# Kernel optimization log

Hardware: AMD Instinct MI355X
Metric: run time of the kernel (lower is better)

The kernel has to match this reference:

```python
import jax, jax.numpy as jnp
import numpy as np

D, H, L, E, K, FF, VIS, NC, NT = 1024, 8, 4, 4, 2, 2048, 1536, 4, 4
HD = D // H


def layer_norm(x, g, b, eps=1e-5):
    m = x.mean(-1, keepdims=True)
    v = ((x - m) ** 2).mean(-1, keepdims=True)
    return (x - m) / jnp.sqrt(v + eps) * g + b


def sinusoidal_pos(seq_len):
    pos = jnp.arange(seq_len, dtype=jnp.float32)[:, None]
    div = jnp.exp(jnp.arange(0, D, 2, dtype=jnp.float32) * (-jnp.log(10000.0) / D))
    pe = jnp.zeros((seq_len, D), dtype=jnp.float32)
    pe = pe.at[:, 0::2].set(jnp.sin(pos * div))
    pe = pe.at[:, 1::2].set(jnp.cos(pos * div))
    return pe


def mha(x, wi, bi, wo, bo):
    # wi: [D, 3D] (pre-transposed), wo: [D, D]
    B, S, _ = x.shape
    qkv = x @ wi + bi
    q, k, v = jnp.split(qkv, 3, axis=-1)
    split = lambda t: t.reshape(B, S, H, HD).transpose(0, 2, 1, 3)
    q, k, v = split(q), split(k), split(v)
    scores = jnp.einsum('bhqd,bhkd->bhqk', q, k) / jnp.sqrt(jnp.float32(HD))
    a = jax.nn.softmax(scores, axis=-1)
    o = jnp.einsum('bhqk,bhkd->bhqd', a, v).transpose(0, 2, 1, 3).reshape(B, S, D)
    return o @ wo + bo


def moe(x_flat, rw, rb, w1, b1, w2, b2):
    # x_flat: [N, D]; rw: [D, E]; w1: [E, D, FF]; w2: [E, FF, D]
    logits = x_flat @ rw + rb                      # [N, E]
    topv, topi = jax.lax.top_k(logits, K)          # [N, K]
    probs = jax.nn.softmax(topv, axis=-1)          # softmax over the top-k logits
    onehot = jax.nn.one_hot(topi, E, dtype=x_flat.dtype)      # [N, K, E]
    combine = jnp.einsum('nk,nke->ne', probs, onehot)         # [N, E]
    h = jax.nn.relu(jnp.einsum('nd,edf->enf', x_flat, w1) + b1[:, None, :])  # [E, N, FF]
    o = jnp.einsum('enf,efd->end', h, w2) + b2[:, None, :]                   # [E, N, D]
    return jnp.einsum('ne,end->nd', combine, o)


def setup_inputs() -> dict:
    key = jax.random.key(0)
    ks = iter(jax.random.split(key, 32))
    s = 0.02
    n = lambda shape: jax.random.normal(next(ks), shape, dtype=jnp.float32) * s
    inp = {
        'vis_feat': jax.random.normal(next(ks), (64, 128, VIS), dtype=jnp.float32),
        'proj_w': n((VIS, D)), 'proj_b': jnp.zeros((D,), jnp.float32),
        'in_proj_w': n((L, D, 3 * D)), 'in_proj_b': jnp.zeros((L, 3 * D), jnp.float32),
        'out_proj_w': n((L, D, D)), 'out_proj_b': jnp.zeros((L, D), jnp.float32),
        'ln1_g': jnp.ones((L, D), jnp.float32), 'ln1_b': jnp.zeros((L, D), jnp.float32),
        'ln2_g': jnp.ones((L, D), jnp.float32), 'ln2_b': jnp.zeros((L, D), jnp.float32),
        'router_w': n((L, D, E)), 'router_b': jnp.zeros((L, E), jnp.float32),
        'ew1': n((L, E, D, FF)), 'eb1': jnp.zeros((L, E, FF), jnp.float32),
        'ew2': n((L, E, FF, D)), 'eb2': jnp.zeros((L, E, D), jnp.float32),
        'attn_w': n((D, 1)), 'attn_b': jnp.zeros((1,), jnp.float32),
        'heads_w': n((NT, D, NC)), 'heads_b': jnp.zeros((NT, NC), jnp.float32),
    }
    return inp


def reference(vis_feat, proj_w, proj_b, in_proj_w, in_proj_b, out_proj_w, out_proj_b,
              ln1_g, ln1_b, ln2_g, ln2_b, router_w, router_b, ew1, eb1, ew2, eb2,
              attn_w, attn_b, heads_w, heads_b):
    B, S, _ = vis_feat.shape
    x = vis_feat @ proj_w + proj_b            # projection to d_model=1024
    x = x + sinusoidal_pos(S)[None]           # positional encoding
    for l in range(L):                         # 4 MoE transformer layers
        x = layer_norm(x + mha(x, in_proj_w[l], in_proj_b[l], out_proj_w[l], out_proj_b[l]),
                       ln1_g[l], ln1_b[l])
        moe_out = moe(x.reshape(B * S, D), router_w[l], router_b[l],
                      ew1[l], eb1[l], ew2[l], eb2[l]).reshape(B, S, D)
        x = layer_norm(x + moe_out, ln2_g[l], ln2_b[l])
    # attention pooling over time, then 4 task heads
    scores = jax.nn.softmax(x @ attn_w + attn_b, axis=1)   # [B, S, 1]
    pooled = jnp.sum(scores * x, axis=1)                   # [B, D]
    logits = jnp.einsum('bd,tdc->tbc', pooled, heads_w) + heads_b[:, None, :]  # [4, B, 4]
    return logits
```

## Files before the change

### kernel.cpp

```cpp
#include <hip/hip_runtime.h>
#include <hip/hip_bf16.h>

typedef unsigned short u16;
typedef unsigned int u32;
using short8 = __attribute__((ext_vector_type(8))) short;
using f32x4  = __attribute__((ext_vector_type(4))) float;

__device__ __forceinline__ u16 f2bu(float f) {
  u32 u = __builtin_bit_cast(u32, f);
  u32 r = u + 0x7fffu + ((u >> 16) & 1u);
  return (u16)(r >> 16);
}
__device__ __forceinline__ float bu2f(u16 u) {
  u32 x = ((u32)u) << 16;
  return __builtin_bit_cast(float, x);
}
__device__ __forceinline__ float waveRedSum(float v) {
  #pragma unroll
  for (int off = 32; off > 0; off >>= 1) v += __shfl_xor(v, off, 64);
  return v;
}
__device__ __forceinline__ void gload16(const void* g, void* l) {
  __builtin_amdgcn_global_load_lds((const __attribute__((address_space(1))) u32*)g,
                                   (__attribute__((address_space(3))) u32*)l, 16, 0, 0);
}

template<int MODE>
__global__ __launch_bounds__(256) void gemm_bt(
    const u16* __restrict__ A, const u16* __restrict__ Bt, const float* __restrict__ bias,
    float* __restrict__ Cf, u16* __restrict__ Cb, u16* __restrict__ M0, u16* __restrict__ M1,
    const int* __restrict__ tok, const float* __restrict__ prob, const int* __restrict__ slot,
    const int* __restrict__ poff, const int* __restrict__ cnts,
    int N, int K)
{
  const int gx = gridDim.x;
  const int nwg = gx * gridDim.y;
  int lid = blockIdx.y * gx + blockIdx.x;
  lid = (lid & 7) * (nwg >> 3) + (lid >> 3);
  const int brow = (lid / gx) << 7, bcol = (lid % gx) << 7;

  int e = 0, rowEnd = 0;
  const u16* Bw = Bt;
  const float* bw = bias;
  if constexpr (MODE >= 2) {
    if (brow >= poff[4]) return;
    #pragma unroll
    for (int q = 1; q < 4; ++q) if (brow >= poff[q]) e = q;
    rowEnd = poff[e] + cnts[e];
    Bw = Bt + (size_t)e * N * K;
    bw = bias + e * N;
  }

  __shared__ __align__(16) u16 As[128 * 32];
  __shared__ __align__(16) u16 Bs[128 * 32];
  const int tid = threadIdx.x;
  const int wave = tid >> 6, lane = tid & 63;
  const int wr = wave >> 1, wc = wave & 1;
  const int r = lane & 15, kg = lane >> 4;

  f32x4 acc[4][4];
  #pragma unroll
  for (int m = 0; m < 4; ++m)
    #pragma unroll
    for (int n = 0; n < 4; ++n) acc[m][n] = f32x4{0.f, 0.f, 0.f, 0.f};

  const int c0 = (wave << 6) + lane;
  const int row0 = c0 >> 2, col0 = (c0 & 3) << 3;
  const int c1 = 256 + c0;
  const int row1 = c1 >> 2, col1 = (c1 & 3) << 3;

  size_t ar0, ar1;
  if constexpr (MODE == 2) {
    const int g0 = brow + row0, g1 = brow + row1;
    ar0 = (size_t)tok[(g0 < rowEnd) ? g0 : poff[e]];
    ar1 = (size_t)tok[(g1 < rowEnd) ? g1 : poff[e]];
  } else {
    ar0 = (size_t)(brow + row0);
    ar1 = (size_t)(brow + row1);
  }
  const u16* Bb = Bw + (size_t)bcol * K;

  for (int k0 = 0; k0 < K; k0 += 32) {
    __syncthreads();
    gload16(A + ar0 * K + k0 + col0, &As[(wave << 6) * 8]);
    gload16(Bb + (size_t)row0 * K + k0 + col0, &Bs[(wave << 6) * 8]);
    gload16(A + ar1 * K + k0 + col1, &As[(256 + (wave << 6)) * 8]);
    gload16(Bb + (size_t)row1 * K + k0 + col1, &Bs[(256 + (wave << 6)) * 8]);
    __syncthreads();
    short8 a[4], b[4];
    #pragma unroll
    for (int m = 0; m < 4; ++m)
      a[m] = *(const short8*)&As[((wr << 6) + (m << 4) + r) * 32 + (kg << 3)];
    #pragma unroll
    for (int n = 0; n < 4; ++n)
      b[n] = *(const short8*)&Bs[((wc << 6) + (n << 4) + r) * 32 + (kg << 3)];
    #pragma unroll
    for (int m = 0; m < 4; ++m)
      #pragma unroll
      for (int n = 0; n < 4; ++n)
        acc[m][n] = __builtin_amdgcn_mfma_f32_16x16x32_bf16(a[m], b[n], acc[m][n], 0, 0, 0);
  }

  if constexpr (MODE == 3) {
    #pragma unroll
    for (int m = 0; m < 4; ++m) {
      #pragma unroll
      for (int i4 = 0; i4 < 4; ++i4) {
        const int row = brow + (wr << 6) + (m << 4) + (kg << 2) + i4;
        if (row < rowEnd) {
          const int t = tok[row];
          const float pp = prob[row];
          u16* dst = slot[row] ? M1 : M0;
          #pragma unroll
          for (int n = 0; n < 4; ++n) {
            const int col = bcol + (wc << 6) + (n << 4) + r;
            dst[(size_t)t * N + col] = f2bu((acc[m][n][i4] + bw[col]) * pp);
          }
        }
      }
    }
  } else {
    #pragma unroll
    for (int m = 0; m < 4; ++m) {
      #pragma unroll
      for (int n = 0; n < 4; ++n) {
        const int col = bcol + (wc << 6) + (n << 4) + r;
        const float bv = bw[col];
        #pragma unroll
        for (int i4 = 0; i4 < 4; ++i4) {
          const int row = brow + (wr << 6) + (m << 4) + (kg << 2) + i4;
          const float v = acc[m][n][i4] + bv;
          const size_t off = (size_t)row * N + col;
          if constexpr (MODE == 0) Cf[off] = v;
          else if constexpr (MODE == 1) Cb[off] = f2bu(v);
          else Cb[off] = f2bu(fmaxf(v, 0.f));
        }
      }
    }
  }
}

__global__ __launch_bounds__(256) void tconv_kernel(const float* __restrict__ src, u16* __restrict__ dst,
                                                    int K, int N)
{
  __shared__ float t[32][33];
  const size_t moff = (size_t)blockIdx.z * K * N;
  const float* s = src + moff;
  u16* d = dst + moff;
  const int n0 = blockIdx.x << 5, k0 = blockIdx.y << 5;
  const int x = threadIdx.x, y = threadIdx.y;
  #pragma unroll
  for (int j = 0; j < 4; ++j) t[y + 8 * j][x] = s[(size_t)(k0 + y + 8 * j) * N + n0 + x];
  __syncthreads();
  #pragma unroll
  for (int j = 0; j < 4; ++j) d[(size_t)(n0 + y + 8 * j) * K + k0 + x] = f2bu(t[x][y + 8 * j]);
}

__global__ __launch_bounds__(256) void conv_kernel(const float* __restrict__ in, u16* __restrict__ out)
{
  const size_t i = ((size_t)blockIdx.x * 256 + threadIdx.x) * 4;
  float4 v = *(const float4*)(in + i);
  *(ushort4*)(out + i) = make_ushort4(f2bu(v.x), f2bu(v.y), f2bu(v.z), f2bu(v.w));
}

__global__ __launch_bounds__(256) void pe_kernel(float* __restrict__ X, u16* __restrict__ Xb)
{
  const int idx = blockIdx.x * 256 + threadIdx.x;
  const int d = idx & 1023;
  const int s = (idx >> 10) & 127;
  const float de = (float)(d & ~1);
  const float ang = (float)s * expf(de * (-9.210340371976184f / 1024.f));
  const float pe = (d & 1) ? cosf(ang) : sinf(ang);
  const float v = X[idx] + pe;
  X[idx] = v;
  Xb[idx] = f2bu(v);
}

__global__ __launch_bounds__(256) void ln_kernel(const float* __restrict__ Xi, const float* __restrict__ R,
    const float* __restrict__ g, const float* __restrict__ be,
    float* __restrict__ Xo, u16* __restrict__ Xbo)
{
  const size_t base = (size_t)blockIdx.x << 10;
  const int tid = threadIdx.x;
  float vals[4]; float s = 0.f, s2 = 0.f;
  #pragma unroll
  for (int j = 0; j < 4; ++j) {
    const int d = tid + (j << 8);
    const float v = Xi[base + d] + R[base + d];
    vals[j] = v; s += v; s2 += v * v;
  }
  s = waveRedSum(s); s2 = waveRedSum(s2);
  __shared__ float rs[4], rs2[4];
  const int wave = tid >> 6, lane = tid & 63;
  if (lane == 0) { rs[wave] = s; rs2[wave] = s2; }
  __syncthreads();
  s = rs[0] + rs[1] + rs[2] + rs[3];
  s2 = rs2[0] + rs2[1] + rs2[2] + rs2[3];
  const float mean = s * (1.f / 1024.f);
  const float var = s2 * (1.f / 1024.f) - mean * mean;
  const float inv = rsqrtf(var + 1e-5f);
  #pragma unroll
  for (int j = 0; j < 4; ++j) {
    const int d = tid + (j << 8);
    const float y = (vals[j] - mean) * inv * g[d] + be[d];
    Xo[base + d] = y;
    Xbo[base + d] = f2bu(y);
  }
}

__global__ __launch_bounds__(256) void ln2_kernel(const float* __restrict__ Xi,
    const u16* __restrict__ R0, const u16* __restrict__ R1,
    const float* __restrict__ g, const float* __restrict__ be,
    float* __restrict__ Xo, u16* __restrict__ Xbo)
{
  const size_t base = (size_t)blockIdx.x << 10;
  const int tid = threadIdx.x;
  float vals[4]; float s = 0.f, s2 = 0.f;
  #pragma unroll
  for (int j = 0; j < 4; ++j) {
    const int d = tid + (j << 8);
    const float v = Xi[base + d] + (bu2f(R0[base + d]) + bu2f(R1[base + d]));
    vals[j] = v; s += v; s2 += v * v;
  }
  s = waveRedSum(s); s2 = waveRedSum(s2);
  __shared__ float rs[4], rs2[4];
  const int wave = tid >> 6, lane = tid & 63;
  if (lane == 0) { rs[wave] = s; rs2[wave] = s2; }
  __syncthreads();
  s = rs[0] + rs[1] + rs[2] + rs[3];
  s2 = rs2[0] + rs2[1] + rs2[2] + rs2[3];
  const float mean = s * (1.f / 1024.f);
  const float var = s2 * (1.f / 1024.f) - mean * mean;
  const float inv = rsqrtf(var + 1e-5f);
  #pragma unroll
  for (int j = 0; j < 4; ++j) {
    const int d = tid + (j << 8);
    const float y = (vals[j] - mean) * inv * g[d] + be[d];
    Xo[base + d] = y;
    Xbo[base + d] = f2bu(y);
  }
}

#define LDW 136
__global__ __launch_bounds__(256) void attn_mfma_kernel(const u16* __restrict__ QKVb, u16* __restrict__ ATTb)
{
  __shared__ __align__(16) u16 Kb[128 * LDW];
  __shared__ __align__(16) u16 Vt[128 * LDW];
  __shared__ __align__(16) u16 Pb[128 * LDW];
  const int b = blockIdx.x >> 3, h = blockIdx.x & 7;
  const int tid = threadIdx.x;
  const int wave = tid >> 6, lane = tid & 63;
  const int r = lane & 15, kg = lane >> 4;
  const u16* base = QKVb + (size_t)b * 128 * 3072 + h * 128;

  for (int i = tid; i < 128 * 16; i += 256) {
    const int row = i >> 4, c8 = (i & 15) << 3;
    *(short8*)&Kb[row * LDW + c8] = *(const short8*)(base + (size_t)row * 3072 + 1024 + c8);
  }
  for (int i = tid; i < 128 * 128; i += 256) {
    const int d = i & 127, key = i >> 7;
    Vt[d * LDW + key] = base[(size_t)key * 3072 + 2048 + d];
  }

  short8 a[2][4];
  #pragma unroll
  for (int m = 0; m < 2; ++m) {
    const int row = wave * 32 + m * 16 + r;
    const u16* qp = base + (size_t)row * 3072;
    #pragma unroll
    for (int ks = 0; ks < 4; ++ks)
      a[m][ks] = *(const short8*)(qp + ks * 32 + kg * 8);
  }
  __syncthreads();

  f32x4 acc[2][8];
  #pragma unroll
  for (int m = 0; m < 2; ++m)
    #pragma unroll
    for (int n = 0; n < 8; ++n) acc[m][n] = f32x4{0.f, 0.f, 0.f, 0.f};
  #pragma unroll
  for (int n = 0; n < 8; ++n) {
    #pragma unroll
    for (int ks = 0; ks < 4; ++ks) {
      short8 bf = *(const short8*)&Kb[(n * 16 + r) * LDW + ks * 32 + kg * 8];
      #pragma unroll
      for (int m = 0; m < 2; ++m)
        acc[m][n] = __builtin_amdgcn_mfma_f32_16x16x32_bf16(a[m][ks], bf, acc[m][n], 0, 0, 0);
    }
  }

  const float sc = 0.08838834764831845f;
  #pragma unroll
  for (int m = 0; m < 2; ++m) {
    #pragma unroll
    for (int i = 0; i < 4; ++i) {
      float mx = -1e30f;
      #pragma unroll
      for (int n = 0; n < 8; ++n) mx = fmaxf(mx, acc[m][n][i]);
      #pragma unroll
      for (int msk = 1; msk < 16; msk <<= 1) mx = fmaxf(mx, __shfl_xor(mx, msk, 64));
      float s = 0.f;
      #pragma unroll
      for (int n = 0; n < 8; ++n) { float pv = __expf((acc[m][n][i] - mx) * sc); acc[m][n][i] = pv; s += pv; }
      #pragma unroll
      for (int msk = 1; msk < 16; msk <<= 1) s += __shfl_xor(s, msk, 64);
      const float inv = 1.f / s;
      #pragma unroll
      for (int n = 0; n < 8; ++n) {
        const int prow = wave * 32 + m * 16 + kg * 4 + i;
        Pb[prow * LDW + n * 16 + r] = f2bu(acc[m][n][i] * inv);
      }
    }
  }

  f32x4 oacc[2][8];
  #pragma unroll
  for (int m = 0; m < 2; ++m)
    #pragma unroll
    for (int n = 0; n < 8; ++n) oacc[m][n] = f32x4{0.f, 0.f, 0.f, 0.f};
  #pragma unroll
  for (int ks = 0; ks < 4; ++ks) {
    short8 pa[2];
    #pragma unroll
    for (int m = 0; m < 2; ++m)
      pa[m] = *(const short8*)&Pb[(wave * 32 + m * 16 + r) * LDW + ks * 32 + kg * 8];
    #pragma unroll
    for (int n = 0; n < 8; ++n) {
      short8 vb = *(const short8*)&Vt[(n * 16 + r) * LDW + ks * 32 + kg * 8];
      #pragma unroll
      for (int m = 0; m < 2; ++m)
        oacc[m][n] = __builtin_amdgcn_mfma_f32_16x16x32_bf16(pa[m], vb, oacc[m][n], 0, 0, 0);
    }
  }

  u16* op = ATTb + ((size_t)b * 128) * 1024 + h * 128;
  #pragma unroll
  for (int m = 0; m < 2; ++m) {
    #pragma unroll
    for (int n = 0; n < 8; ++n) {
      #pragma unroll
      for (int i = 0; i < 4; ++i) {
        const int row = wave * 32 + m * 16 + kg * 4 + i;
        op[(size_t)row * 1024 + n * 16 + r] = f2bu(oacc[m][n][i]);
      }
    }
  }
}
#undef LDW

__global__ __launch_bounds__(256) void router_kernel(const float* __restrict__ X, const float* __restrict__ rw,
    const float* __restrict__ rb, int* __restrict__ choice, float* __restrict__ prob2)
{
  const int token = blockIdx.x * 4 + (threadIdx.x >> 6);
  const int lane = threadIdx.x & 63;
  const float* xp = X + ((size_t)token << 10);
  float a0 = 0, a1 = 0, a2 = 0, a3 = 0;
  #pragma unroll
  for (int j = 0; j < 16; ++j) {
    const int k = lane + (j << 6);
    const float x = xp[k];
    const float4 w = *(const float4*)(rw + ((size_t)k << 2));
    a0 += x * w.x; a1 += x * w.y; a2 += x * w.z; a3 += x * w.w;
  }
  a0 = waveRedSum(a0); a1 = waveRedSum(a1); a2 = waveRedSum(a2); a3 = waveRedSum(a3);
  if (lane == 0) {
    float v[4] = {a0 + rb[0], a1 + rb[1], a2 + rb[2], a3 + rb[3]};
    int i1 = 0;
    for (int e = 1; e < 4; ++e) if (v[e] > v[i1]) i1 = e;
    int i2 = (i1 == 0) ? 1 : 0;
    for (int e = 0; e < 4; ++e) if (e != i1 && v[e] > v[i2]) i2 = e;
    const float p2 = __expf(v[i2] - v[i1]);
    const float is = 1.f / (1.f + p2);
    choice[token] = i1 | (i2 << 8);
    prob2[token * 2]     = is;
    prob2[token * 2 + 1] = p2 * is;
  }
}

__global__ __launch_bounds__(256) void build_lists_kernel(
    const int* __restrict__ choice, const float* __restrict__ prob2,
    int* __restrict__ cnt, int* __restrict__ poff,
    int* __restrict__ tok, float* __restrict__ prob, int* __restrict__ slot)
{
  const int tid = threadIdx.x;
  __shared__ int sc[256];
  __shared__ int basev;
  if (tid == 0) basev = 0;
  __syncthreads();
  for (int e = 0; e < 4; ++e) {
    const int t0 = tid << 5;
    int code[32]; int mycount = 0;
    #pragma unroll
    for (int j = 0; j < 32; ++j) {
      const int c = choice[t0 + j];
      const int m = ((c & 255) == e) ? 1 : (((c >> 8) == e) ? 2 : 0);
      code[j] = m;
      mycount += (m != 0);
    }
    sc[tid] = mycount;
    __syncthreads();
    for (int off = 1; off < 256; off <<= 1) {
      const int add = (tid >= off) ? sc[tid - off] : 0;
      __syncthreads();
      sc[tid] += add;
      __syncthreads();
    }
    const int total = sc[255];
    const int start = basev;
    int pos = start + sc[tid] - mycount;
    #pragma unroll
    for (int j = 0; j < 32; ++j) {
      if (code[j]) {
        const int token = t0 + j;
        tok[pos] = token;
        prob[pos] = prob2[token * 2 + (code[j] - 1)];
        slot[pos] = code[j] - 1;
        ++pos;
      }
    }
    __syncthreads();
    if (tid == 0) {
      cnt[e] = total;
      poff[e] = start;
      basev = start + ((total + 255) & ~255);
      if (e == 3) poff[4] = basev;
    }
    __syncthreads();
  }
}

__global__ __launch_bounds__(256) void score_kernel(const float* __restrict__ X, const float* __restrict__ aw,
    const float* __restrict__ ab, float* __restrict__ S)
{
  const int token = blockIdx.x * 4 + (threadIdx.x >> 6);
  const int lane = threadIdx.x & 63;
  const float* xp = X + ((size_t)token << 10);
  float s = 0.f;
  #pragma unroll
  for (int j = 0; j < 16; ++j) { const int k = lane + (j << 6); s += xp[k] * aw[k]; }
  s = waveRedSum(s);
  if (lane == 0) S[token] = s + ab[0];
}

__global__ __launch_bounds__(256) void pool_kernel(const float* __restrict__ X, const float* __restrict__ S,
                                                   float* __restrict__ P)
{
  const int b = blockIdx.x;
  const int tid = threadIdx.x;
  __shared__ float p[128];
  if (tid < 128) p[tid] = S[b * 128 + tid];
  __syncthreads();
  float mx = -1e30f;
  for (int t = 0; t < 128; ++t) mx = fmaxf(mx, p[t]);
  float sum = 0.f;
  for (int t = 0; t < 128; ++t) sum += __expf(p[t] - mx);
  const float inv = 1.f / sum;
  __syncthreads();
  if (tid < 128) p[tid] = __expf(p[tid] - mx) * inv;
  __syncthreads();
  float acc[4] = {0.f, 0.f, 0.f, 0.f};
  for (int t = 0; t < 128; ++t) {
    const float pt = p[t];
    const float* xp = X + ((size_t)(b * 128 + t) << 10) + tid;
    #pragma unroll
    for (int j = 0; j < 4; ++j) acc[j] += pt * xp[j << 8];
  }
  #pragma unroll
  for (int j = 0; j < 4; ++j) P[((size_t)b << 10) + tid + (j << 8)] = acc[j];
}

__global__ __launch_bounds__(256) void heads_kernel(const float* __restrict__ P, const float* __restrict__ hw,
    const float* __restrict__ hb, float* __restrict__ out)
{
  const int idx = blockIdx.x * 4 + (threadIdx.x >> 6);
  const int lane = threadIdx.x & 63;
  const int t = idx >> 8, b = (idx >> 2) & 63, c = idx & 3;
  const float* pp = P + ((size_t)b << 10);
  const float* wp = hw + (size_t)t * 4096 + c;
  float s = 0.f;
  #pragma unroll
  for (int j = 0; j < 16; ++j) { const int k = lane + (j << 6); s += pp[k] * wp[(size_t)k << 2]; }
  s = waveRedSum(s);
  if (lane == 0) out[idx] = s + hb[t * 4 + c];
}

extern "C" void kernel_launch(void* const* d_in, const int* in_sizes, int n_in,
                              void* d_out, int out_size, void* d_ws, size_t ws_size,
                              hipStream_t stream)
{
  (void)in_sizes; (void)n_in; (void)out_size; (void)ws_size;
  const float* vis        = (const float*)d_in[0];
  const float* proj_w     = (const float*)d_in[1];
  const float* proj_b     = (const float*)d_in[2];
  const float* in_proj_w  = (const float*)d_in[3];
  const float* in_proj_b  = (const float*)d_in[4];
  const float* out_proj_w = (const float*)d_in[5];
  const float* out_proj_b = (const float*)d_in[6];
  const float* ln1_g      = (const float*)d_in[7];
  const float* ln1_b      = (const float*)d_in[8];
  const float* ln2_g      = (const float*)d_in[9];
  const float* ln2_b      = (const float*)d_in[10];
  const float* router_w   = (const float*)d_in[11];
  const float* router_b   = (const float*)d_in[12];
  const float* ew1        = (const float*)d_in[13];
  const float* eb1        = (const float*)d_in[14];
  const float* ew2        = (const float*)d_in[15];
  const float* eb2        = (const float*)d_in[16];
  const float* attn_w     = (const float*)d_in[17];
  const float* attn_b     = (const float*)d_in[18];
  const float* heads_w    = (const float*)d_in[19];
  const float* heads_b    = (const float*)d_in[20];
  float* out = (float*)d_out;

  char* p = (char*)d_ws;
  auto take = [&](size_t bytes) -> char* {
    char* q = p; p += (bytes + 255) & ~(size_t)255; return q;
  };
  float* X    = (float*)take(8192ULL * 1024 * 4);
  u16*   Xb   = (u16*)  take(8192ULL * 1024 * 2);
  char*  QKVr = take(104857600ULL);
  u16*   ATTb = (u16*)  take(8192ULL * 1024 * 2);
  int*   CNT  = (int*)  take(4 * 4);
  int*   POFF = (int*)  take(5 * 4);
  int*   CHOICE = (int*)take(8192ULL * 4);
  float* PROB2  = (float*)take(8192ULL * 2 * 4);
  int*   TOK  = (int*)  take(17408ULL * 4);
  float* PROB = (float*)take(17408ULL * 4);
  int*   SLOT = (int*)  take(17408ULL * 4);
  float* S    = (float*)take(8192ULL * 4);
  float* POOL = (float*)take(64ULL * 1024 * 4);
  u16*   Wqkv = (u16*)  take(3072ULL * 1024 * 2);
  u16*   Wout = (u16*)  take(1024ULL * 1024 * 2);
  u16*   We1  = (u16*)  take(4ULL * 2048 * 1024 * 2);
  u16*   We2  = (u16*)  take(4ULL * 1024 * 2048 * 2);
  u16*   QKVb  = (u16*)QKVr;
  float* O     = (float*)QKVr;
  u16*   H     = (u16*)QKVr;
  u16*   MOE0b = (u16*)(QKVr + 71303168);
  u16*   MOE1b = (u16*)(QKVr + 71303168 + 16777216);
  u16*   Wproj = We1;
  u16*   VISb  = (u16*)QKVr;

  const dim3 tb(32, 8);
  #define GARGS Cf_, Cb_, MOE0b, MOE1b, TOK, PROB, SLOT, POFF, CNT

  tconv_kernel<<<dim3(1024 / 32, 1536 / 32, 1), tb, 0, stream>>>(proj_w, Wproj, 1536, 1024);
  conv_kernel<<<(8192 * 1536 / 4) / 256, 256, 0, stream>>>(vis, VISb);
  {
    float* Cf_ = X; u16* Cb_ = nullptr;
    gemm_bt<0><<<dim3(8, 64), 256, 0, stream>>>(VISb, Wproj, proj_b, GARGS, 1024, 1536);
  }
  pe_kernel<<<8192 * 1024 / 256, 256, 0, stream>>>(X, Xb);

  for (int l = 0; l < 4; ++l) {
    tconv_kernel<<<dim3(3072 / 32, 1024 / 32, 1), tb, 0, stream>>>(in_proj_w + (size_t)l * 1024 * 3072, Wqkv, 1024, 3072);
    tconv_kernel<<<dim3(1024 / 32, 1024 / 32, 1), tb, 0, stream>>>(out_proj_w + (size_t)l * 1024 * 1024, Wout, 1024, 1024);
    tconv_kernel<<<dim3(2048 / 32, 1024 / 32, 4), tb, 0, stream>>>(ew1 + (size_t)l * 4 * 1024 * 2048, We1, 1024, 2048);
    tconv_kernel<<<dim3(1024 / 32, 2048 / 32, 4), tb, 0, stream>>>(ew2 + (size_t)l * 4 * 2048 * 1024, We2, 2048, 1024);

    {
      float* Cf_ = nullptr; u16* Cb_ = QKVb;
      gemm_bt<1><<<dim3(24, 64), 256, 0, stream>>>(Xb, Wqkv, in_proj_b + l * 3072, GARGS, 3072, 1024);
    }
    attn_mfma_kernel<<<512, 256, 0, stream>>>(QKVb, ATTb);
    {
      float* Cf_ = O; u16* Cb_ = nullptr;
      gemm_bt<0><<<dim3(8, 64), 256, 0, stream>>>(ATTb, Wout, out_proj_b + l * 1024, GARGS, 1024, 1024);
    }
    ln_kernel<<<8192, 256, 0, stream>>>(X, O, ln1_g + l * 1024, ln1_b + l * 1024, X, Xb);

    router_kernel<<<2048, 256, 0, stream>>>(X, router_w + l * 4096, router_b + l * 4, CHOICE, PROB2);
    build_lists_kernel<<<1, 256, 0, stream>>>(CHOICE, PROB2, CNT, POFF, TOK, PROB, SLOT);
    {
      float* Cf_ = nullptr; u16* Cb_ = H;
      gemm_bt<2><<<dim3(16, 136), 256, 0, stream>>>(Xb, We1, eb1 + (size_t)l * 4 * 2048, GARGS, 2048, 1024);
    }
    {
      float* Cf_ = nullptr; u16* Cb_ = nullptr;
      gemm_bt<3><<<dim3(8, 136), 256, 0, stream>>>(H, We2, eb2 + (size_t)l * 4 * 1024, GARGS, 1024, 2048);
    }
    ln2_kernel<<<8192, 256, 0, stream>>>(X, MOE0b, MOE1b, ln2_g + l * 1024, ln2_b + l * 1024, X, Xb);
  }

  score_kernel<<<2048, 256, 0, stream>>>(X, attn_w, attn_b, S);
  pool_kernel<<<64, 256, 0, stream>>>(X, S, POOL);
  heads_kernel<<<256, 256, 0, stream>>>(POOL, heads_w, heads_b, out);
  #undef GARGS
}
```

Before: 1.964 ms.

## Fuse router and score into layernorm kernels, bf16 out-proj output, parallel list build

The router logits and top-2 selection are computed inside the post-attention layernorm kernel, and the pooling score dot product is folded into the last layer's second layernorm. This removes two separate kernels that each re-read the full activation tensor. The out-projection GEMM now writes bf16 instead of fp32, halving that intermediate's traffic at some precision cost. build_lists now uses one wave per expert with shuffle-based scans instead of four sequential block-wide scans with many barriers.

```diff
diff --git a/kernel.cpp b/kernel.cpp
--- a/kernel.cpp
+++ b/kernel.cpp
@@ -176,21 +176,25 @@
   Xb[idx] = f2bu(v);
 }
 
-__global__ __launch_bounds__(256) void ln_kernel(const float* __restrict__ Xi, const float* __restrict__ R,
+__global__ __launch_bounds__(256) void ln_kernel(const float* __restrict__ Xi, const u16* __restrict__ R,
     const float* __restrict__ g, const float* __restrict__ be,
-    float* __restrict__ Xo, u16* __restrict__ Xbo)
-{
-  const size_t base = (size_t)blockIdx.x << 10;
+    const float* __restrict__ rw, const float* __restrict__ rb,
+    float* __restrict__ Xo, u16* __restrict__ Xbo,
+    int* __restrict__ choice, float* __restrict__ prob2)
+{
+  const int token = blockIdx.x;
+  const size_t base = (size_t)token << 10;
   const int tid = threadIdx.x;
   float vals[4]; float s = 0.f, s2 = 0.f;
   #pragma unroll
   for (int j = 0; j < 4; ++j) {
     const int d = tid + (j << 8);
-    const float v = Xi[base + d] + R[base + d];
+    const float v = Xi[base + d] + bu2f(R[base + d]);
     vals[j] = v; s += v; s2 += v * v;
   }
   s = waveRedSum(s); s2 = waveRedSum(s2);
   __shared__ float rs[4], rs2[4];
+  __shared__ float rl[4][4];
   const int wave = tid >> 6, lane = tid & 63;
   if (lane == 0) { rs[wave] = s; rs2[wave] = s2; }
   __syncthreads();
@@ -199,21 +203,44 @@
   const float mean = s * (1.f / 1024.f);
   const float var = s2 * (1.f / 1024.f) - mean * mean;
   const float inv = rsqrtf(var + 1e-5f);
+  float l0 = 0.f, l1 = 0.f, l2 = 0.f, l3 = 0.f;
   #pragma unroll
   for (int j = 0; j < 4; ++j) {
     const int d = tid + (j << 8);
     const float y = (vals[j] - mean) * inv * g[d] + be[d];
     Xo[base + d] = y;
     Xbo[base + d] = f2bu(y);
+    const float4 w = *(const float4*)(rw + ((size_t)d << 2));
+    l0 += y * w.x; l1 += y * w.y; l2 += y * w.z; l3 += y * w.w;
+  }
+  l0 = waveRedSum(l0); l1 = waveRedSum(l1); l2 = waveRedSum(l2); l3 = waveRedSum(l3);
+  if (lane == 0) { rl[wave][0] = l0; rl[wave][1] = l1; rl[wave][2] = l2; rl[wave][3] = l3; }
+  __syncthreads();
+  if (tid == 0) {
+    float v[4];
+    #pragma unroll
+    for (int q = 0; q < 4; ++q)
+      v[q] = rl[0][q] + rl[1][q] + rl[2][q] + rl[3][q] + rb[q];
+    int i1 = 0;
+    for (int q = 1; q < 4; ++q) if (v[q] > v[i1]) i1 = q;
+    int i2 = (i1 == 0) ? 1 : 0;
+    for (int q = 0; q < 4; ++q) if (q != i1 && v[q] > v[i2]) i2 = q;
+    const float p2 = __expf(v[i2] - v[i1]);
+    const float is = 1.f / (1.f + p2);
+    choice[token] = i1 | (i2 << 8);
+    prob2[token * 2]     = is;
+    prob2[token * 2 + 1] = p2 * is;
   }
 }
 
 __global__ __launch_bounds__(256) void ln2_kernel(const float* __restrict__ Xi,
     const u16* __restrict__ R0, const u16* __restrict__ R1,
     const float* __restrict__ g, const float* __restrict__ be,
-    float* __restrict__ Xo, u16* __restrict__ Xbo)
-{
-  const size_t base = (size_t)blockIdx.x << 10;
+    float* __restrict__ Xo, u16* __restrict__ Xbo,
+    const float* __restrict__ aw, const float* __restrict__ ab, float* __restrict__ S)
+{
+  const int token = blockIdx.x;
+  const size_t base = (size_t)token << 10;
   const int tid = threadIdx.x;
   float vals[4]; float s = 0.f, s2 = 0.f;
   #pragma unroll
@@ -224,6 +251,7 @@
   }
   s = waveRedSum(s); s2 = waveRedSum(s2);
   __shared__ float rs[4], rs2[4];
+  __shared__ float rsc[4];
   const int wave = tid >> 6, lane = tid & 63;
   if (lane == 0) { rs[wave] = s; rs2[wave] = s2; }
   __syncthreads();
@@ -232,12 +260,20 @@
   const float mean = s * (1.f / 1024.f);
   const float var = s2 * (1.f / 1024.f) - mean * mean;
   const float inv = rsqrtf(var + 1e-5f);
+  float sc = 0.f;
   #pragma unroll
   for (int j = 0; j < 4; ++j) {
     const int d = tid + (j << 8);
     const float y = (vals[j] - mean) * inv * g[d] + be[d];
     Xo[base + d] = y;
     Xbo[base + d] = f2bu(y);
+    if (aw) sc += y * aw[d];
+  }
+  if (aw) {
+    sc = waveRedSum(sc);
+    if (lane == 0) rsc[wave] = sc;
+    __syncthreads();
+    if (tid == 0) S[token] = rsc[0] + rsc[1] + rsc[2] + rsc[3] + ab[0];
   }
 }
 
@@ -348,98 +384,49 @@
 }
 #undef LDW
 
-__global__ __launch_bounds__(256) void router_kernel(const float* __restrict__ X, const float* __restrict__ rw,
-    const float* __restrict__ rb, int* __restrict__ choice, float* __restrict__ prob2)
-{
-  const int token = blockIdx.x * 4 + (threadIdx.x >> 6);
-  const int lane = threadIdx.x & 63;
-  const float* xp = X + ((size_t)token << 10);
-  float a0 = 0, a1 = 0, a2 = 0, a3 = 0;
-  #pragma unroll
-  for (int j = 0; j < 16; ++j) {
-    const int k = lane + (j << 6);
-    const float x = xp[k];
-    const float4 w = *(const float4*)(rw + ((size_t)k << 2));
-    a0 += x * w.x; a1 += x * w.y; a2 += x * w.z; a3 += x * w.w;
-  }
-  a0 = waveRedSum(a0); a1 = waveRedSum(a1); a2 = waveRedSum(a2); a3 = waveRedSum(a3);
-  if (lane == 0) {
-    float v[4] = {a0 + rb[0], a1 + rb[1], a2 + rb[2], a3 + rb[3]};
-    int i1 = 0;
-    for (int e = 1; e < 4; ++e) if (v[e] > v[i1]) i1 = e;
-    int i2 = (i1 == 0) ? 1 : 0;
-    for (int e = 0; e < 4; ++e) if (e != i1 && v[e] > v[i2]) i2 = e;
-    const float p2 = __expf(v[i2] - v[i1]);
-    const float is = 1.f / (1.f + p2);
-    choice[token] = i1 | (i2 << 8);
-    prob2[token * 2]     = is;
-    prob2[token * 2 + 1] = p2 * is;
-  }
-}
-
 __global__ __launch_bounds__(256) void build_lists_kernel(
     const int* __restrict__ choice, const float* __restrict__ prob2,
     int* __restrict__ cnt, int* __restrict__ poff,
     int* __restrict__ tok, float* __restrict__ prob, int* __restrict__ slot)
 {
   const int tid = threadIdx.x;
-  __shared__ int sc[256];
-  __shared__ int basev;
-  if (tid == 0) basev = 0;
-  __syncthreads();
-  for (int e = 0; e < 4; ++e) {
-    const int t0 = tid << 5;
-    int code[32]; int mycount = 0;
-    #pragma unroll
-    for (int j = 0; j < 32; ++j) {
-      const int c = choice[t0 + j];
-      const int m = ((c & 255) == e) ? 1 : (((c >> 8) == e) ? 2 : 0);
-      code[j] = m;
-      mycount += (m != 0);
-    }
-    sc[tid] = mycount;
-    __syncthreads();
-    for (int off = 1; off < 256; off <<= 1) {
-      const int add = (tid >= off) ? sc[tid - off] : 0;
-      __syncthreads();
-      sc[tid] += add;
-      __syncthreads();
-    }
-    const int total = sc[255];
-    const int start = basev;
-    int pos = start + sc[tid] - mycount;
-    #pragma unroll
-    for (int j = 0; j < 32; ++j) {
-      if (code[j]) {
-        const int token = t0 + j;
-        tok[pos] = token;
-        prob[pos] = prob2[token * 2 + (code[j] - 1)];
-        slot[pos] = code[j] - 1;
-        ++pos;
-      }
-    }
-    __syncthreads();
-    if (tid == 0) {
-      cnt[e] = total;
-      poff[e] = start;
-      basev = start + ((total + 255) & ~255);
-      if (e == 3) poff[4] = basev;
-    }
-    __syncthreads();
-  }
-}
-
-__global__ __launch_bounds__(256) void score_kernel(const float* __restrict__ X, const float* __restrict__ aw,
-    const float* __restrict__ ab, float* __restrict__ S)
-{
-  const int token = blockIdx.x * 4 + (threadIdx.x >> 6);
-  const int lane = threadIdx.x & 63;
-  const float* xp = X + ((size_t)token << 10);
-  float s = 0.f;
-  #pragma unroll
-  for (int j = 0; j < 16; ++j) { const int k = lane + (j << 6); s += xp[k] * aw[k]; }
-  s = waveRedSum(s);
-  if (lane == 0) S[token] = s + ab[0];
+  const int e = tid >> 6, lane = tid & 63;
+  const int t0 = lane << 7;
+  int mycount = 0;
+  for (int j = 0; j < 128; ++j) {
+    const int c = choice[t0 + j];
+    mycount += (((c & 255) == e) || ((c >> 8) == e)) ? 1 : 0;
+  }
+  int incl = mycount;
+  #pragma unroll
+  for (int off = 1; off < 64; off <<= 1) {
+    const int t = __shfl_up(incl, off, 64);
+    if (lane >= off) incl += t;
+  }
+  __shared__ int totals[4];
+  if (lane == 63) totals[e] = incl;
+  __syncthreads();
+  int base = 0;
+  #pragma unroll
+  for (int q = 0; q < 4; ++q)
+    if (q < e) base += (totals[q] + 255) & ~255;
+  int pos = base + incl - mycount;
+  for (int j = 0; j < 128; ++j) {
+    const int token = t0 + j;
+    const int c = choice[token];
+    const int m = ((c & 255) == e) ? 1 : (((c >> 8) == e) ? 2 : 0);
+    if (m) {
+      tok[pos] = token;
+      prob[pos] = prob2[token * 2 + (m - 1)];
+      slot[pos] = m - 1;
+      ++pos;
+    }
+  }
+  if (lane == 0) {
+    cnt[e] = totals[e];
+    poff[e] = base;
+    if (e == 3) poff[4] = base + ((totals[3] + 255) & ~255);
+  }
 }
 
 __global__ __launch_bounds__(256) void pool_kernel(const float* __restrict__ X, const float* __restrict__ S,
@@ -534,7 +521,7 @@
   u16*   We1  = (u16*)  take(4ULL * 2048 * 1024 * 2);
   u16*   We2  = (u16*)  take(4ULL * 1024 * 2048 * 2);
   u16*   QKVb  = (u16*)QKVr;
-  float* O     = (float*)QKVr;
+  u16*   O16   = (u16*)QKVr;
   u16*   H     = (u16*)QKVr;
   u16*   MOE0b = (u16*)(QKVr + 71303168);
   u16*   MOE1b = (u16*)(QKVr + 71303168 + 16777216);
@@ -564,12 +551,12 @@
     }
     attn_mfma_kernel<<<512, 256, 0, stream>>>(QKVb, ATTb);
     {
-      float* Cf_ = O; u16* Cb_ = nullptr;
-      gemm_bt<0><<<dim3(8, 64), 256, 0, stream>>>(ATTb, Wout, out_proj_b + l * 1024, GARGS, 1024, 1024);
-    }
-    ln_kernel<<<8192, 256, 0, stream>>>(X, O, ln1_g + l * 1024, ln1_b + l * 1024, X, Xb);
-
-    router_kernel<<<2048, 256, 0, stream>>>(X, router_w + l * 4096, router_b + l * 4, CHOICE, PROB2);
+      float* Cf_ = nullptr; u16* Cb_ = O16;
+      gemm_bt<1><<<dim3(8, 64), 256, 0, stream>>>(ATTb, Wout, out_proj_b + l * 1024, GARGS, 1024, 1024);
+    }
+    ln_kernel<<<8192, 256, 0, stream>>>(X, O16, ln1_g + l * 1024, ln1_b + l * 1024,
+                                        router_w + (size_t)l * 4096, router_b + l * 4,
+                                        X, Xb, CHOICE, PROB2);
     build_lists_kernel<<<1, 256, 0, stream>>>(CHOICE, PROB2, CNT, POFF, TOK, PROB, SLOT);
     {
       float* Cf_ = nullptr; u16* Cb_ = H;
@@ -579,10 +566,10 @@
       float* Cf_ = nullptr; u16* Cb_ = nullptr;
       gemm_bt<3><<<dim3(8, 136), 256, 0, stream>>>(H, We2, eb2 + (size_t)l * 4 * 1024, GARGS, 1024, 2048);
     }
-    ln2_kernel<<<8192, 256, 0, stream>>>(X, MOE0b, MOE1b, ln2_g + l * 1024, ln2_b + l * 1024, X, Xb);
-  }
-
-  score_kernel<<<2048, 256, 0, stream>>>(X, attn_w, attn_b, S);
+    ln2_kernel<<<8192, 256, 0, stream>>>(X, MOE0b, MOE1b, ln2_g + l * 1024, ln2_b + l * 1024,
+                                         X, Xb, (l == 3) ? attn_w : nullptr, attn_b, S);
+  }
+
   pool_kernel<<<64, 256, 0, stream>>>(X, S, POOL);
   heads_kernel<<<256, 256, 0, stream>>>(POOL, heads_w, heads_b, out);
   #undef GARGS
```

Measured after the change: 2.003 ms. No clear change (+2.0%).
